# Optimization experiments

Hardware: AMD Instinct MI355X
Metric: run time of the kernel (lower is better)

## Reference

```python
import jax, jax.numpy as jnp
import numpy as np
from jax import lax

JITTER = 1e-6


def setup_inputs() -> dict:
    key = jax.random.key(0)
    ks = jax.random.split(key, 8)
    T, sd, od = 2048, 128, 64
    y = jax.random.normal(ks[0], (T, od), dtype=jnp.float32)
    # stable transition: spectral radius < 1
    A = jax.random.normal(ks[1], (sd, sd), dtype=jnp.float32) * (0.9 / np.sqrt(sd))
    C = jax.random.normal(ks[2], (od, sd), dtype=jnp.float32) / np.sqrt(sd)
    # SPD noise covariances
    Bq = jax.random.normal(ks[3], (sd, sd), dtype=jnp.float32)
    Q = (Bq @ Bq.T) / sd * 0.1 + 0.01 * jnp.eye(sd, dtype=jnp.float32)
    Br = jax.random.normal(ks[4], (od, od), dtype=jnp.float32)
    R = (Br @ Br.T) / od * 0.1 + 0.01 * jnp.eye(od, dtype=jnp.float32)
    z0 = jax.random.normal(ks[5], (sd,), dtype=jnp.float32)
    P0 = jnp.eye(sd, dtype=jnp.float32)
    return {"y": y, "A": A, "C": C, "Q": Q, "R": R, "z0": z0, "P0": P0}


def _kf(y, A, C, Q, R, z0, P0):
    sd = A.shape[0]
    od = C.shape[0]
    dt = y.dtype
    I_s = jnp.eye(sd, dtype=dt)
    jit_o = JITTER * jnp.eye(od, dtype=dt)
    log2pi = jnp.log(jnp.asarray(2.0 * np.pi, dtype=dt))

    def update(z_pred, P_pred, y_t):
        nan_mask = jnp.isnan(y_t)
        valid = ~jnp.any(nan_mask)
        y_safe = jnp.where(nan_mask, 0.0, y_t)
        innov = y_safe - C @ z_pred                      # (od,)
        S = C @ P_pred @ C.T + R + jit_o                 # S_stable (od, od)
        PCt = P_pred @ C.T                               # (sd, od)
        K = jnp.linalg.solve(S.T, PCt.T).T               # (sd, od)
        z_u = z_pred + K @ innov
        I_KC = I_s - K @ C
        P_u = I_KC @ P_pred @ I_KC.T + K @ R @ K.T
        _, logdet = jnp.linalg.slogdet(S)
        quad = innov @ jnp.linalg.solve(S, innov)
        ll_inc = -0.5 * (logdet + quad + od * log2pi)
        z = jnp.where(valid, z_u, z_pred)
        P = jnp.where(valid, P_u, P_pred)
        ll_inc = jnp.where(valid, ll_inc, jnp.zeros((), dt))
        return z, P, ll_inc

    # t = 0: no predict step, use (z0, P0) directly
    z_0, P_0, ll0 = update(z0, P0, y[0])

    def step(carry, y_t):
        z, P, ll = carry
        z_pred = A @ z
        P_pred = A @ P @ A.T + Q
        z_n, P_n, ll_inc = update(z_pred, P_pred, y_t)
        return (z_n, P_n, ll + ll_inc), (z_n, P_n)

    (_, _, log_likelihood), (zs, Ps) = lax.scan(step, (z_0, P_0, ll0), y[1:])
    states = jnp.concatenate([z_0[None], zs], axis=0)           # (T, sd)
    covariances = jnp.concatenate([P_0[None], Ps], axis=0)      # (T, sd, sd)
    return states, covariances, log_likelihood


def reference(y, A, C, Q, R, z0, P0):
    return _kf(y, A, C, Q, R, z0, P0)
```

## Files before the change

### kernel.cpp

```cpp
#include <hip/hip_runtime.h>
#include <math.h>

#define NTH 1024
#define SD 128
#define OD 64
#define PST 130
#define SST 65

#define OFF_P     0
#define OFF_T     16640
#define OFF_PCTT  16640
#define OFF_S     24960
#define OFF_L     29120
#define OFF_LINV  24960
#define OFF_KT    24960
#define OFF_SINV  33280
#define OFF_Z     37440
#define OFF_T1    37568
#define OFF_INNOV 37760
#define OFF_RED   37824
#define OFF_MISC  37888
#define LDS_FLOATS 37896

#define WS_LL    1
#define WS_LOGD  2
#define WS_Z     128
#define WS_KT    1024
#define WS_SINV  10240
#define WS_CA    16384
#define WS_QUAD  24576

#define LCH  32
#define WARM 160

#define LOG2PI_F 1.8378770664093453f
#define FREEZE_TOL 1e-5f

__launch_bounds__(NTH)
__global__ void kf_seq(const float* __restrict__ y, const float* __restrict__ A,
                       const float* __restrict__ C, const float* __restrict__ Q,
                       const float* __restrict__ R, const float* __restrict__ z0,
                       const float* __restrict__ P0, float* __restrict__ out,
                       int T, float* __restrict__ wsf, int* __restrict__ wsi) {
  extern __shared__ float lds[];
  const int tid = (int)threadIdx.x;
  const int ti = tid >> 5, tj = tid & 31;
  float* states = out;
  float* cov = out + (size_t)T * SD;

  for (int p = 0; p < 16; ++p) {
    int idx = tid + p * NTH;
    lds[OFF_P + (idx >> 7) * PST + (idx & 127)] = P0[idx];
  }
  if (tid < SD) lds[OFF_Z + tid] = z0[tid];
  if (tid == 0) { lds[OFF_MISC + 0] = 0.f; lds[OFF_MISC + 1] = 0.f; }
  __syncthreads();

  {
    int bad = 0;
    int n4 = (T * OD) >> 2;
    for (int idx = tid; idx < n4; idx += NTH) {
      float4 v = ((const float4*)y)[idx];
      if (v.x != v.x || v.y != v.y || v.z != v.z || v.w != v.w) bad = 1;
    }
    if (bad) lds[OFF_MISC + 1] = 1.f;
  }
  __syncthreads();
  const bool hasNaN = (lds[OFF_MISC + 1] != 0.f);

  float llacc = 0.f;
  float logdet_cur = 0.f;
  int tF = T;

  for (int t = 0; t < T; ++t) {
    if (t > 0) {
      {
        const int i0 = ti * 4, j0 = tj * 4;
        float acc[4][4] = {};
        for (int k = 0; k < SD; ++k) {
          float av[4], bv[4];
#pragma unroll
          for (int r = 0; r < 4; ++r) av[r] = A[(i0 + r) * SD + k];
#pragma unroll
          for (int c = 0; c < 4; ++c) bv[c] = lds[OFF_P + k * PST + j0 + c];
#pragma unroll
          for (int r = 0; r < 4; ++r)
#pragma unroll
            for (int c = 0; c < 4; ++c) acc[r][c] += av[r] * bv[c];
        }
        __syncthreads();
#pragma unroll
        for (int r = 0; r < 4; ++r)
#pragma unroll
          for (int c = 0; c < 4; ++c)
            lds[OFF_T + (i0 + r) * PST + j0 + c] = acc[r][c];
      }
      __syncthreads();
      {
        const int i0 = ti * 4, j0 = tj * 4;
        float acc[4][4] = {};
        for (int k = 0; k < SD; ++k) {
          float av[4], xv[4];
#pragma unroll
          for (int r = 0; r < 4; ++r) av[r] = A[(i0 + r) * SD + k];
#pragma unroll
          for (int c = 0; c < 4; ++c) xv[c] = lds[OFF_T + (j0 + c) * PST + k];
#pragma unroll
          for (int r = 0; r < 4; ++r)
#pragma unroll
            for (int c = 0; c < 4; ++c) acc[r][c] += av[r] * xv[c];
        }
#pragma unroll
        for (int r = 0; r < 4; ++r)
#pragma unroll
          for (int c = 0; c < 4; ++c)
            lds[OFF_P + (i0 + r) * PST + j0 + c] =
                acc[r][c] + Q[(i0 + r) * SD + j0 + c];
      }
      {
        int i = tid >> 3, s = tid & 7;
        float sum = 0.f;
        for (int kk = 0; kk < 16; ++kk) {
          int k = s * 16 + kk;
          sum += A[i * SD + k] * lds[OFF_Z + k];
        }
        sum += __shfl_xor(sum, 1);
        sum += __shfl_xor(sum, 2);
        sum += __shfl_xor(sum, 4);
        if (s == 0) lds[OFF_T1 + i] = sum;
      }
      if (tid == 0) lds[OFF_MISC + 2] = 1.f;
      __syncthreads();
    } else {
      if (tid < SD) lds[OFF_T1 + tid] = lds[OFF_Z + tid];
      if (tid == 0) lds[OFF_MISC + 2] = 1.f;
      __syncthreads();
    }

    {
      const int a0 = ti * 2, i0 = tj * 4;
      float acc[2][4] = {};
      for (int m = 0; m < SD; ++m) {
        float c0 = C[(a0 + 0) * SD + m];
        float c1 = C[(a0 + 1) * SD + m];
        float pv[4];
#pragma unroll
        for (int c = 0; c < 4; ++c) pv[c] = lds[OFF_P + m * PST + i0 + c];
#pragma unroll
        for (int c = 0; c < 4; ++c) { acc[0][c] += c0 * pv[c]; acc[1][c] += c1 * pv[c]; }
      }
#pragma unroll
      for (int r = 0; r < 2; ++r)
#pragma unroll
        for (int c = 0; c < 4; ++c)
          lds[OFF_PCTT + (a0 + r) * PST + i0 + c] = acc[r][c];
      if (tid < OD) {
        float yv = y[(size_t)t * OD + tid];
        if (yv != yv) lds[OFF_MISC + 2] = 0.f;
      }
    }
    __syncthreads();

    {
      const int a0 = ti * 2, b0 = tj * 2;
      float acc[2][2] = {};
      for (int k = 0; k < SD; ++k) {
        float c0 = C[(a0 + 0) * SD + k];
        float c1 = C[(a0 + 1) * SD + k];
        float p0 = lds[OFF_PCTT + (b0 + 0) * PST + k];
        float p1 = lds[OFF_PCTT + (b0 + 1) * PST + k];
        acc[0][0] += c0 * p0; acc[0][1] += c0 * p1;
        acc[1][0] += c1 * p0; acc[1][1] += c1 * p1;
      }
#pragma unroll
      for (int r = 0; r < 2; ++r)
#pragma unroll
        for (int c = 0; c < 2; ++c) {
          int a = a0 + r, b = b0 + c;
          lds[OFF_S + a * SST + b] =
              acc[r][c] + R[a * OD + b] + ((a == b) ? 1e-6f : 0.f);
        }
    }
    if (tid < 512) {
      int o = tid >> 3, s = tid & 7;
      float sum = 0.f;
      for (int kk = 0; kk < 16; ++kk) {
        int k = s * 16 + kk;
        sum += C[o * SD + k] * lds[OFF_T1 + k];
      }
      sum += __shfl_xor(sum, 1);
      sum += __shfl_xor(sum, 2);
      sum += __shfl_xor(sum, 4);
      if (s == 0) {
        float yv = y[(size_t)t * OD + o];
        if (yv != yv) yv = 0.f;
        lds[OFF_INNOV + o] = yv - sum;
      }
    }
    __syncthreads();

    float logdet_step = 0.f;
    for (int j = 0; j < OD; ++j) {
      float a = lds[OFF_S + j * SST + j];
      float inva = 1.0f / a;
      float irs = rsqrtf(a);
      if (tid == 0) logdet_step += logf(a);
#pragma unroll
      for (int p = 0; p < 4; ++p) {
        int idx = tid + p * NTH;
        int i = idx >> 6, k = idx & 63;
        if (i > j && k > j)
          lds[OFF_S + i * SST + k] -=
              lds[OFF_S + i * SST + j] * lds[OFF_S + k * SST + j] * inva;
        if (k == j && i >= j)
          lds[OFF_L + i * SST + j] = lds[OFF_S + i * SST + j] * irs;
      }
      __syncthreads();
    }
    if (tid == 0) logdet_cur = logdet_step;

    if (tid < OD) {
      int c = tid;
      for (int i = 0; i < c; ++i) lds[OFF_LINV + i * SST + c] = 0.f;
      for (int i = c; i < OD; ++i) {
        float s = (i == c) ? 1.f : 0.f;
        for (int j = c; j < i; ++j)
          s -= lds[OFF_L + i * SST + j] * lds[OFF_LINV + j * SST + c];
        lds[OFF_LINV + i * SST + c] = s / lds[OFF_L + i * SST + i];
      }
    }
    __syncthreads();

    {
      const int a0 = ti * 2, b0 = tj * 2;
      float acc[2][2] = {};
      for (int k = 0; k < OD; ++k) {
        float la0 = lds[OFF_LINV + k * SST + a0 + 0];
        float la1 = lds[OFF_LINV + k * SST + a0 + 1];
        float lb0 = lds[OFF_LINV + k * SST + b0 + 0];
        float lb1 = lds[OFF_LINV + k * SST + b0 + 1];
        acc[0][0] += la0 * lb0; acc[0][1] += la0 * lb1;
        acc[1][0] += la1 * lb0; acc[1][1] += la1 * lb1;
      }
#pragma unroll
      for (int r = 0; r < 2; ++r)
#pragma unroll
        for (int c = 0; c < 2; ++c)
          lds[OFF_SINV + (a0 + r) * SST + b0 + c] = acc[r][c];
    }
    __syncthreads();

    if (tid < 512) {
      int o = tid >> 3, s = tid & 7;
      float sum = 0.f;
      for (int kk = 0; kk < 8; ++kk) {
        int k = s * 8 + kk;
        sum += lds[OFF_SINV + o * SST + k] * lds[OFF_INNOV + k];
      }
      sum += __shfl_xor(sum, 1);
      sum += __shfl_xor(sum, 2);
      sum += __shfl_xor(sum, 4);
      if (s == 0) lds[OFF_RED + o] = sum * lds[OFF_INNOV + o];
    }
    {
      const int a0 = ti * 2, i0 = tj * 4;
      float acc[2][4] = {};
      for (int b = 0; b < OD; ++b) {
        float s0 = lds[OFF_SINV + (a0 + 0) * SST + b];
        float s1 = lds[OFF_SINV + (a0 + 1) * SST + b];
        float pv[4];
#pragma unroll
        for (int c = 0; c < 4; ++c) pv[c] = lds[OFF_PCTT + b * PST + i0 + c];
#pragma unroll
        for (int c = 0; c < 4; ++c) { acc[0][c] += s0 * pv[c]; acc[1][c] += s1 * pv[c]; }
      }
      __syncthreads();
#pragma unroll
      for (int r = 0; r < 2; ++r)
#pragma unroll
        for (int c = 0; c < 4; ++c)
          lds[OFF_KT + (a0 + r) * PST + i0 + c] = acc[r][c];
    }
    __syncthreads();

    const bool valid = (lds[OFF_MISC + 2] != 0.f);
    if (tid < 64) {
      float q = lds[OFF_RED + tid];
      q += __shfl_xor(q, 1);  q += __shfl_xor(q, 2);  q += __shfl_xor(q, 4);
      q += __shfl_xor(q, 8);  q += __shfl_xor(q, 16); q += __shfl_xor(q, 32);
      if (tid == 0 && valid)
        llacc += -0.5f * (logdet_step + q + OD * LOG2PI_F);
    }
    {
      int i = tid >> 3, s = tid & 7;
      float sum = 0.f;
      for (int kk = 0; kk < 8; ++kk) {
        int k = s * 8 + kk;
        sum += lds[OFF_KT + k * PST + i] * lds[OFF_INNOV + k];
      }
      sum += __shfl_xor(sum, 1);
      sum += __shfl_xor(sum, 2);
      sum += __shfl_xor(sum, 4);
      if (s == 0) {
        float zi = lds[OFF_T1 + i] + (valid ? sum : 0.f);
        lds[OFF_Z + i] = zi;
        states[(size_t)t * SD + i] = zi;
      }
    }
    {
      const int i0 = ti * 4, j0 = tj * 4;
      float acc[4][4] = {};
      for (int a = 0; a < OD; ++a) {
        float kv[4], pv[4];
#pragma unroll
        for (int r = 0; r < 4; ++r) kv[r] = lds[OFF_KT + a * PST + i0 + r];
#pragma unroll
        for (int c = 0; c < 4; ++c) pv[c] = lds[OFF_PCTT + a * PST + j0 + c];
#pragma unroll
        for (int r = 0; r < 4; ++r)
#pragma unroll
          for (int c = 0; c < 4; ++c) acc[r][c] += kv[r] * pv[c];
      }
      if (valid) {
#pragma unroll
        for (int r = 0; r < 4; ++r)
#pragma unroll
          for (int c = 0; c < 4; ++c)
            lds[OFF_P + (i0 + r) * PST + j0 + c] -= acc[r][c];
      }
    }
    __syncthreads();

    {
      float maxd = 0.f;
      float* covt = cov + (size_t)t * SD * SD;
      const float* covp = cov + (size_t)(t - 1) * SD * SD;
#pragma unroll
      for (int p = 0; p < 4; ++p) {
        int idx = tid + p * NTH;
        int base = idx * 4;
        int i = base >> 7, j = base & 127;
        float v0 = lds[OFF_P + i * PST + j + 0];
        float v1 = lds[OFF_P + i * PST + j + 1];
        float v2 = lds[OFF_P + i * PST + j + 2];
        float v3 = lds[OFF_P + i * PST + j + 3];
        covt[base + 0] = v0; covt[base + 1] = v1;
        covt[base + 2] = v2; covt[base + 3] = v3;
        if (t > 0 && !hasNaN) {
          float4 pv = ((const float4*)covp)[idx];
          maxd = fmaxf(maxd, fmaxf(fmaxf(fabsf(v0 - pv.x), fabsf(v1 - pv.y)),
                                   fmaxf(fabsf(v2 - pv.z), fabsf(v3 - pv.w))));
        }
      }
      for (int m = 1; m < 64; m <<= 1) maxd = fmaxf(maxd, __shfl_xor(maxd, m));
      if ((tid & 63) == 0) lds[OFF_RED + (tid >> 6)] = maxd;
    }
    __syncthreads();
    if (tid == 0) {
      float md = 0.f;
      for (int w = 0; w < 16; ++w) md = fmaxf(md, lds[OFF_RED + w]);
      if (t > 0 && !hasNaN && md < FREEZE_TOL) lds[OFF_MISC + 0] = 1.f;
    }
    __syncthreads();
    if (lds[OFF_MISC + 0] != 0.f) { tF = t + 1; break; }
    __syncthreads();
  }

  if (tid == 0) {
    wsi[0] = tF;
    wsf[WS_LL] = llacc;
    wsf[WS_LOGD] = logdet_cur;
  }
  if (tid < SD) wsf[WS_Z + tid] = lds[OFF_Z + tid];
  if (tF < T) {
    for (int p = 0; p < 8; ++p) {
      int idx = tid + p * NTH;
      int a = idx >> 7, i = idx & 127;
      wsf[WS_KT + idx] = lds[OFF_KT + a * PST + i];
    }
    for (int p = 0; p < 4; ++p) {
      int idx = tid + p * NTH;
      int a = idx >> 6, b = idx & 63;
      wsf[WS_SINV + idx] = lds[OFF_SINV + a * SST + b];
    }
    __syncthreads();
    for (int p = 0; p < 16; ++p) {
      int idx = tid + p * NTH;
      lds[OFF_P + (idx >> 7) * PST + (idx & 127)] = A[idx];
    }
    __syncthreads();
    {
      const int a0 = ti * 2, k0 = tj * 4;
      float acc[2][4] = {};
      for (int m = 0; m < SD; ++m) {
        float c0 = C[(a0 + 0) * SD + m];
        float c1 = C[(a0 + 1) * SD + m];
        float av[4];
#pragma unroll
        for (int cc = 0; cc < 4; ++cc) av[cc] = lds[OFF_P + m * PST + k0 + cc];
#pragma unroll
        for (int cc = 0; cc < 4; ++cc) { acc[0][cc] += c0 * av[cc]; acc[1][cc] += c1 * av[cc]; }
      }
#pragma unroll
      for (int rr = 0; rr < 2; ++rr)
#pragma unroll
        for (int cc = 0; cc < 4; ++cc)
          wsf[WS_CA + (a0 + rr) * SD + k0 + cc] = acc[rr][cc];
    }
  }
}

__launch_bounds__(512, 1)
__global__ void kf_chunk(const float* __restrict__ y, const float* __restrict__ A,
                         const float* __restrict__ wsf, const int* __restrict__ wsi,
                         float* __restrict__ out, int T) {
  __shared__ __align__(16) float zv[SD];
  __shared__ __align__(16) float vv[192];
  __shared__ __align__(16) float yb[2][OD];
  __shared__ float red[8];
  const int tid = (int)threadIdx.x;
  const int c = (int)blockIdx.x;
  const int tF = wsi[0];
  float* states = out;
  float* quad_out = (float*)wsf + WS_QUAD;

  int t_end = (c + 1) * LCH; if (t_end > T) t_end = T;
  int t_begin = c * LCH; if (t_begin < tF) t_begin = tF;
  float qacc = 0.f;

  if (t_begin < t_end) {
    int s0 = t_begin - WARM; if (s0 < tF) s0 = tF;
    const int r = tid >> 1, h = tid & 1;
    const int ki = tid >> 2, kq = tid & 3;
    const int so = tid >> 3, se = tid & 7;

    float G[64];
    if (tid < 384) {
      const float* src = (r < SD) ? (A + r * SD + h * 64)
                                  : (wsf + WS_CA + (r - SD) * SD + h * 64);
#pragma unroll
      for (int k = 0; k < 16; ++k) {
        float4 g4 = ((const float4*)src)[k];
        G[4 * k + 0] = g4.x; G[4 * k + 1] = g4.y;
        G[4 * k + 2] = g4.z; G[4 * k + 3] = g4.w;
      }
    }
    float K[16];
#pragma unroll
    for (int k = 0; k < 16; ++k) K[k] = wsf[WS_KT + (kq * 16 + k) * SD + ki];
    float Sv[8];
#pragma unroll
    for (int k = 0; k < 8; ++k) Sv[k] = wsf[WS_SINV + so * OD + se * 8 + k];

    if (tid < SD) zv[tid] = (s0 == tF) ? wsf[WS_Z + tid] : 0.f;
    if (tid < OD) yb[s0 & 1][tid] = y[(size_t)s0 * OD + tid];
    __syncthreads();

    for (int t = s0; t < t_end; ++t) {
      if (tid < 384) {
        const float* zz = zv + h * 64;
        float sum = 0.f;
#pragma unroll
        for (int k = 0; k < 16; ++k) {
          float4 z4 = ((const float4*)zz)[k];
          sum += G[4 * k + 0] * z4.x + G[4 * k + 1] * z4.y +
                 G[4 * k + 2] * z4.z + G[4 * k + 3] * z4.w;
        }
        sum += __shfl_xor(sum, 1);
        if (h == 0) vv[r] = sum;
      } else if (tid >= 448) {
        int o = tid - 448;
        if (t + 1 < t_end) yb[(t + 1) & 1][o] = y[(size_t)(t + 1) * OD + o];
      }
      __syncthreads();
      const float* ybt = yb[t & 1];
      {
        const int a0 = kq * 16;
        float sum = 0.f;
#pragma unroll
        for (int k4 = 0; k4 < 4; ++k4) {
          float4 y4 = ((const float4*)(ybt + a0))[k4];
          float4 v4 = ((const float4*)(vv + SD + a0))[k4];
          sum += K[4 * k4 + 0] * (y4.x - v4.x) + K[4 * k4 + 1] * (y4.y - v4.y) +
                 K[4 * k4 + 2] * (y4.z - v4.z) + K[4 * k4 + 3] * (y4.w - v4.w);
        }
        sum += __shfl_xor(sum, 1);
        sum += __shfl_xor(sum, 2);
        if (kq == 0) {
          float zi = vv[ki] + sum;
          zv[ki] = zi;
          if (t >= t_begin) states[(size_t)t * SD + ki] = zi;
        }
      }
      if (t >= t_begin) {
        const int b0 = se * 8;
        float sp = 0.f;
#pragma unroll
        for (int k4 = 0; k4 < 2; ++k4) {
          float4 y4 = ((const float4*)(ybt + b0))[k4];
          float4 v4 = ((const float4*)(vv + SD + b0))[k4];
          sp += Sv[4 * k4 + 0] * (y4.x - v4.x) + Sv[4 * k4 + 1] * (y4.y - v4.y) +
                Sv[4 * k4 + 2] * (y4.z - v4.z) + Sv[4 * k4 + 3] * (y4.w - v4.w);
        }
        qacc += sp * (ybt[so] - vv[SD + so]);
      }
      __syncthreads();
    }
  }

  float q = qacc;
  for (int m = 1; m < 64; m <<= 1) q += __shfl_xor(q, m);
  if ((tid & 63) == 0) red[tid >> 6] = q;
  __syncthreads();
  if (tid == 0) {
    float s = 0.f;
    for (int w = 0; w < 8; ++w) s += red[w];
    quad_out[c] = s;
  }
}

__global__ void kf_ll(const float* __restrict__ wsf, const int* __restrict__ wsi,
                      float* __restrict__ out, int T, int nchunks) {
  if (threadIdx.x == 0 && blockIdx.x == 0) {
    int tF = wsi[0];
    float ll = wsf[WS_LL];
    if (tF < T) {
      float qs = 0.f;
      for (int c = 0; c < nchunks; ++c) qs += wsf[WS_QUAD + c];
      ll += -0.5f * (qs + (float)(T - tF) * (wsf[WS_LOGD] + (float)OD * LOG2PI_F));
    }
    out[(size_t)T * SD + (size_t)T * SD * SD] = ll;
  }
}

__global__ void kf_fill(float* __restrict__ cov, const int* __restrict__ ws_tf, int T) {
  int t = (int)blockIdx.x;
  int tF = ws_tf[0];
  if (t < tF) return;
  const float4* src = (const float4*)(cov + (size_t)(tF - 1) * SD * SD);
  float4* dst = (float4*)(cov + (size_t)t * SD * SD);
#pragma unroll
  for (int p = 0; p < 16; ++p) {
    int idx = (int)threadIdx.x + p * 256;
    dst[idx] = src[idx];
  }
}

extern "C" void kernel_launch(void* const* d_in, const int* in_sizes, int n_in,
                              void* d_out, int out_size, void* d_ws, size_t ws_size,
                              hipStream_t stream) {
  const float* y  = (const float*)d_in[0];
  const float* A  = (const float*)d_in[1];
  const float* C  = (const float*)d_in[2];
  const float* Q  = (const float*)d_in[3];
  const float* R  = (const float*)d_in[4];
  const float* z0 = (const float*)d_in[5];
  const float* P0 = (const float*)d_in[6];
  float* out = (float*)d_out;
  int T = in_sizes[0] / OD;
  float* wsf = (float*)d_ws;
  int* wsi = (int*)d_ws;

  size_t ldsBytes = (size_t)LDS_FLOATS * sizeof(float);
  (void)hipFuncSetAttribute((const void*)kf_seq,
                            hipFuncAttributeMaxDynamicSharedMemorySize,
                            (int)ldsBytes);

  kf_seq<<<dim3(1), dim3(NTH), ldsBytes, stream>>>(y, A, C, Q, R, z0, P0, out, T, wsf, wsi);

  int nch = (T + LCH - 1) / LCH;
  kf_chunk<<<dim3(nch), dim3(512), 0, stream>>>(y, A, wsf, wsi, out, T);
  kf_ll<<<dim3(1), dim3(64), 0, stream>>>(wsf, wsi, out, T, nch);

  float* cov = out + (size_t)T * SD;
  kf_fill<<<dim3(T), dim3(256), 0, stream>>>(cov, wsi, T);
}
```

Measured before the change: 3.798 ms.

## Replace explicit S inverse with in-wave Cholesky and triangular solves for gain

The Cholesky factorization of S now runs within a single wavefront using wave barriers, replacing the 64 block-wide __syncthreads steps. The explicit L-inverse and S-inverse matrix products are dropped; the Kalman gain and the S^-1 innovation are obtained by forward/back substitution on 129 right-hand-side columns. S^-1 is formed only on the frozen-tail path. The inner GEMM loops are also vectorized with float4 LDS and global loads, using a padded row stride of 132. This trades many block barriers and extra matmuls for serial triangular solves on fewer threads.

```diff
diff --git a/kernel.cpp b/kernel.cpp
--- a/kernel.cpp
+++ b/kernel.cpp
@@ -4,23 +4,18 @@
 #define NTH 1024
 #define SD 128
 #define OD 64
-#define PST 130
+#define PST 132
 #define SST 65
 
 #define OFF_P     0
-#define OFF_T     16640
-#define OFF_PCTT  16640
-#define OFF_S     24960
-#define OFF_L     29120
-#define OFF_LINV  24960
-#define OFF_KT    24960
-#define OFF_SINV  33280
-#define OFF_Z     37440
-#define OFF_T1    37568
-#define OFF_INNOV 37760
-#define OFF_RED   37824
-#define OFF_MISC  37888
-#define LDS_FLOATS 37896
+#define OFF_T     16896
+#define OFF_S     33792
+#define OFF_Z     37952
+#define OFF_T1    38080
+#define OFF_INNOV 38208
+#define OFF_RED   38272
+#define OFF_MISC  38336
+#define LDS_FLOATS 38344
 
 #define WS_LL    1
 #define WS_LOGD  2
@@ -70,6 +65,7 @@
 
   float llacc = 0.f;
   float logdet_cur = 0.f;
+  float logdet_step = 0.f;
   int tF = T;
 
   for (int t = 0; t < T; ++t) {
@@ -77,45 +73,61 @@
       {
         const int i0 = ti * 4, j0 = tj * 4;
         float acc[4][4] = {};
-        for (int k = 0; k < SD; ++k) {
-          float av[4], bv[4];
-#pragma unroll
-          for (int r = 0; r < 4; ++r) av[r] = A[(i0 + r) * SD + k];
-#pragma unroll
-          for (int c = 0; c < 4; ++c) bv[c] = lds[OFF_P + k * PST + j0 + c];
+        for (int k = 0; k < SD; k += 4) {
+          float a_[4][4], p_[4][4];
+#pragma unroll
+          for (int r = 0; r < 4; ++r) {
+            float4 v = *(const float4*)&A[(i0 + r) * SD + k];
+            a_[r][0] = v.x; a_[r][1] = v.y; a_[r][2] = v.z; a_[r][3] = v.w;
+          }
+#pragma unroll
+          for (int kk = 0; kk < 4; ++kk) {
+            float4 v = *(const float4*)&lds[OFF_P + (k + kk) * PST + j0];
+            p_[kk][0] = v.x; p_[kk][1] = v.y; p_[kk][2] = v.z; p_[kk][3] = v.w;
+          }
 #pragma unroll
           for (int r = 0; r < 4; ++r)
 #pragma unroll
-            for (int c = 0; c < 4; ++c) acc[r][c] += av[r] * bv[c];
-        }
-        __syncthreads();
-#pragma unroll
-        for (int r = 0; r < 4; ++r)
-#pragma unroll
-          for (int c = 0; c < 4; ++c)
-            lds[OFF_T + (i0 + r) * PST + j0 + c] = acc[r][c];
+            for (int c = 0; c < 4; ++c)
+#pragma unroll
+              for (int kk = 0; kk < 4; ++kk) acc[r][c] += a_[r][kk] * p_[kk][c];
+        }
+#pragma unroll
+        for (int r = 0; r < 4; ++r) {
+          float4 v = {acc[r][0], acc[r][1], acc[r][2], acc[r][3]};
+          *(float4*)&lds[OFF_T + (i0 + r) * PST + j0] = v;
+        }
       }
       __syncthreads();
       {
         const int i0 = ti * 4, j0 = tj * 4;
         float acc[4][4] = {};
-        for (int k = 0; k < SD; ++k) {
-          float av[4], xv[4];
-#pragma unroll
-          for (int r = 0; r < 4; ++r) av[r] = A[(i0 + r) * SD + k];
-#pragma unroll
-          for (int c = 0; c < 4; ++c) xv[c] = lds[OFF_T + (j0 + c) * PST + k];
+        for (int k = 0; k < SD; k += 4) {
+          float x_[4][4], a_[4][4];
+#pragma unroll
+          for (int r = 0; r < 4; ++r) {
+            float4 v = *(const float4*)&lds[OFF_T + (i0 + r) * PST + k];
+            x_[r][0] = v.x; x_[r][1] = v.y; x_[r][2] = v.z; x_[r][3] = v.w;
+          }
+#pragma unroll
+          for (int c = 0; c < 4; ++c) {
+            float4 v = *(const float4*)&A[(j0 + c) * SD + k];
+            a_[c][0] = v.x; a_[c][1] = v.y; a_[c][2] = v.z; a_[c][3] = v.w;
+          }
 #pragma unroll
           for (int r = 0; r < 4; ++r)
 #pragma unroll
-            for (int c = 0; c < 4; ++c) acc[r][c] += av[r] * xv[c];
-        }
-#pragma unroll
-        for (int r = 0; r < 4; ++r)
-#pragma unroll
-          for (int c = 0; c < 4; ++c)
-            lds[OFF_P + (i0 + r) * PST + j0 + c] =
-                acc[r][c] + Q[(i0 + r) * SD + j0 + c];
+            for (int c = 0; c < 4; ++c)
+#pragma unroll
+              for (int kk = 0; kk < 4; ++kk) acc[r][c] += x_[r][kk] * a_[c][kk];
+        }
+#pragma unroll
+        for (int r = 0; r < 4; ++r) {
+          float4 q4 = *(const float4*)&Q[(i0 + r) * SD + j0];
+          float4 v = {acc[r][0] + q4.x, acc[r][1] + q4.y,
+                      acc[r][2] + q4.z, acc[r][3] + q4.w};
+          *(float4*)&lds[OFF_P + (i0 + r) * PST + j0] = v;
+        }
       }
       {
         int i = tid >> 3, s = tid & 7;
@@ -140,20 +152,30 @@
     {
       const int a0 = ti * 2, i0 = tj * 4;
       float acc[2][4] = {};
-      for (int m = 0; m < SD; ++m) {
-        float c0 = C[(a0 + 0) * SD + m];
-        float c1 = C[(a0 + 1) * SD + m];
-        float pv[4];
-#pragma unroll
-        for (int c = 0; c < 4; ++c) pv[c] = lds[OFF_P + m * PST + i0 + c];
-#pragma unroll
-        for (int c = 0; c < 4; ++c) { acc[0][c] += c0 * pv[c]; acc[1][c] += c1 * pv[c]; }
-      }
-#pragma unroll
-      for (int r = 0; r < 2; ++r)
-#pragma unroll
-        for (int c = 0; c < 4; ++c)
-          lds[OFF_PCTT + (a0 + r) * PST + i0 + c] = acc[r][c];
+      for (int m = 0; m < SD; m += 4) {
+        float c_[2][4], p_[4][4];
+#pragma unroll
+        for (int r = 0; r < 2; ++r) {
+          float4 v = *(const float4*)&C[(a0 + r) * SD + m];
+          c_[r][0] = v.x; c_[r][1] = v.y; c_[r][2] = v.z; c_[r][3] = v.w;
+        }
+#pragma unroll
+        for (int mm = 0; mm < 4; ++mm) {
+          float4 v = *(const float4*)&lds[OFF_P + (m + mm) * PST + i0];
+          p_[mm][0] = v.x; p_[mm][1] = v.y; p_[mm][2] = v.z; p_[mm][3] = v.w;
+        }
+#pragma unroll
+        for (int r = 0; r < 2; ++r)
+#pragma unroll
+          for (int c = 0; c < 4; ++c)
+#pragma unroll
+            for (int mm = 0; mm < 4; ++mm) acc[r][c] += c_[r][mm] * p_[mm][c];
+      }
+#pragma unroll
+      for (int r = 0; r < 2; ++r) {
+        float4 v = {acc[r][0], acc[r][1], acc[r][2], acc[r][3]};
+        *(float4*)&lds[OFF_T + (a0 + r) * PST + i0] = v;
+      }
       if (tid < OD) {
         float yv = y[(size_t)t * OD + tid];
         if (yv != yv) lds[OFF_MISC + 2] = 0.f;
@@ -162,23 +184,34 @@
     __syncthreads();
 
     {
-      const int a0 = ti * 2, b0 = tj * 2;
+      const int a0 = ti * 2;
       float acc[2][2] = {};
-      for (int k = 0; k < SD; ++k) {
-        float c0 = C[(a0 + 0) * SD + k];
-        float c1 = C[(a0 + 1) * SD + k];
-        float p0 = lds[OFF_PCTT + (b0 + 0) * PST + k];
-        float p1 = lds[OFF_PCTT + (b0 + 1) * PST + k];
-        acc[0][0] += c0 * p0; acc[0][1] += c0 * p1;
-        acc[1][0] += c1 * p0; acc[1][1] += c1 * p1;
+      for (int k = 0; k < SD; k += 4) {
+        float pa_[2][4], cb_[2][4];
+#pragma unroll
+        for (int r = 0; r < 2; ++r) {
+          float4 v = *(const float4*)&lds[OFF_T + (a0 + r) * PST + k];
+          pa_[r][0] = v.x; pa_[r][1] = v.y; pa_[r][2] = v.z; pa_[r][3] = v.w;
+        }
+#pragma unroll
+        for (int cb = 0; cb < 2; ++cb) {
+          float4 v = *(const float4*)&C[(tj + 32 * cb) * SD + k];
+          cb_[cb][0] = v.x; cb_[cb][1] = v.y; cb_[cb][2] = v.z; cb_[cb][3] = v.w;
+        }
+#pragma unroll
+        for (int r = 0; r < 2; ++r)
+#pragma unroll
+          for (int cb = 0; cb < 2; ++cb)
+#pragma unroll
+            for (int kk = 0; kk < 4; ++kk) acc[r][cb] += pa_[r][kk] * cb_[cb][kk];
       }
 #pragma unroll
       for (int r = 0; r < 2; ++r)
 #pragma unroll
-        for (int c = 0; c < 2; ++c) {
-          int a = a0 + r, b = b0 + c;
+        for (int cb = 0; cb < 2; ++cb) {
+          int a = a0 + r, b = tj + 32 * cb;
           lds[OFF_S + a * SST + b] =
-              acc[r][c] + R[a * OD + b] + ((a == b) ? 1e-6f : 0.f);
+              acc[r][cb] + R[a * OD + b] + ((a == b) ? 1e-6f : 0.f);
         }
     }
     if (tid < 512) {
@@ -199,104 +232,70 @@
     }
     __syncthreads();
 
-    float logdet_step = 0.f;
-    for (int j = 0; j < OD; ++j) {
-      float a = lds[OFF_S + j * SST + j];
-      float inva = 1.0f / a;
-      float irs = rsqrtf(a);
-      if (tid == 0) logdet_step += logf(a);
-#pragma unroll
-      for (int p = 0; p < 4; ++p) {
-        int idx = tid + p * NTH;
-        int i = idx >> 6, k = idx & 63;
-        if (i > j && k > j)
-          lds[OFF_S + i * SST + k] -=
-              lds[OFF_S + i * SST + j] * lds[OFF_S + k * SST + j] * inva;
-        if (k == j && i >= j)
-          lds[OFF_L + i * SST + j] = lds[OFF_S + i * SST + j] * irs;
-      }
-      __syncthreads();
-    }
-    if (tid == 0) logdet_cur = logdet_step;
-
-    if (tid < OD) {
-      int c = tid;
-      for (int i = 0; i < c; ++i) lds[OFF_LINV + i * SST + c] = 0.f;
-      for (int i = c; i < OD; ++i) {
-        float s = (i == c) ? 1.f : 0.f;
-        for (int j = c; j < i; ++j)
-          s -= lds[OFF_L + i * SST + j] * lds[OFF_LINV + j * SST + c];
-        lds[OFF_LINV + i * SST + c] = s / lds[OFF_L + i * SST + i];
-      }
-    }
-    __syncthreads();
-
-    {
-      const int a0 = ti * 2, b0 = tj * 2;
-      float acc[2][2] = {};
-      for (int k = 0; k < OD; ++k) {
-        float la0 = lds[OFF_LINV + k * SST + a0 + 0];
-        float la1 = lds[OFF_LINV + k * SST + a0 + 1];
-        float lb0 = lds[OFF_LINV + k * SST + b0 + 0];
-        float lb1 = lds[OFF_LINV + k * SST + b0 + 1];
-        acc[0][0] += la0 * lb0; acc[0][1] += la0 * lb1;
-        acc[1][0] += la1 * lb0; acc[1][1] += la1 * lb1;
-      }
-#pragma unroll
-      for (int r = 0; r < 2; ++r)
-#pragma unroll
-        for (int c = 0; c < 2; ++c)
-          lds[OFF_SINV + (a0 + r) * SST + b0 + c] = acc[r][c];
-    }
-    __syncthreads();
-
-    if (tid < 512) {
-      int o = tid >> 3, s = tid & 7;
-      float sum = 0.f;
-      for (int kk = 0; kk < 8; ++kk) {
-        int k = s * 8 + kk;
-        sum += lds[OFF_SINV + o * SST + k] * lds[OFF_INNOV + k];
-      }
-      sum += __shfl_xor(sum, 1);
-      sum += __shfl_xor(sum, 2);
-      sum += __shfl_xor(sum, 4);
-      if (s == 0) lds[OFF_RED + o] = sum * lds[OFF_INNOV + o];
-    }
-    {
-      const int a0 = ti * 2, i0 = tj * 4;
-      float acc[2][4] = {};
-      for (int b = 0; b < OD; ++b) {
-        float s0 = lds[OFF_SINV + (a0 + 0) * SST + b];
-        float s1 = lds[OFF_SINV + (a0 + 1) * SST + b];
-        float pv[4];
-#pragma unroll
-        for (int c = 0; c < 4; ++c) pv[c] = lds[OFF_PCTT + b * PST + i0 + c];
-#pragma unroll
-        for (int c = 0; c < 4; ++c) { acc[0][c] += s0 * pv[c]; acc[1][c] += s1 * pv[c]; }
-      }
-      __syncthreads();
-#pragma unroll
-      for (int r = 0; r < 2; ++r)
-#pragma unroll
-        for (int c = 0; c < 4; ++c)
-          lds[OFF_KT + (a0 + r) * PST + i0 + c] = acc[r][c];
+    logdet_step = 0.f;
+    if (tid < 64) {
+      const int i = tid;
+      for (int j = 0; j < OD; ++j) {
+        float p = lds[OFF_S + j * SST + j];
+        float inv = 1.0f / p;
+        float sij = (i > j) ? lds[OFF_S + i * SST + j] : 0.f;
+        for (int k = j + 1; k <= i; ++k) {
+          float skj = lds[OFF_S + k * SST + j];
+          lds[OFF_S + i * SST + k] -= sij * skj * inv;
+        }
+        __builtin_amdgcn_wave_barrier();
+        if (i > j) lds[OFF_S + i * SST + j] = sij * rsqrtf(p);
+        else if (i == j) lds[OFF_S + j * SST + j] = sqrtf(p);
+        if (i == 0) logdet_step += logf(p);
+        __builtin_amdgcn_wave_barrier();
+      }
+    }
+    __syncthreads();
+
+    if (tid < 129) {
+      const int c = tid;
+      const int xb = OFF_T + 64 * PST + c;
+      for (int i = 0; i < OD; ++i) {
+        float s0 = (c < SD) ? lds[OFF_T + i * PST + c] : lds[OFF_INNOV + i];
+        float s1 = 0.f;
+        int j = 0;
+        for (; j + 1 < i; j += 2) {
+          s0 -= lds[OFF_S + i * SST + j]     * lds[xb + j * PST];
+          s1 -= lds[OFF_S + i * SST + j + 1] * lds[xb + (j + 1) * PST];
+        }
+        if (j < i) s0 -= lds[OFF_S + i * SST + j] * lds[xb + j * PST];
+        lds[xb + i * PST] = (s0 + s1) / lds[OFF_S + i * SST + i];
+      }
+      for (int i = OD - 1; i >= 0; --i) {
+        float s0 = lds[xb + i * PST];
+        float s1 = 0.f;
+        int j = i + 1;
+        for (; j + 1 < OD; j += 2) {
+          s0 -= lds[OFF_S + j * SST + i]       * lds[xb + j * PST];
+          s1 -= lds[OFF_S + (j + 1) * SST + i] * lds[xb + (j + 1) * PST];
+        }
+        if (j < OD) s0 -= lds[OFF_S + j * SST + i] * lds[xb + j * PST];
+        lds[xb + i * PST] = (s0 + s1) / lds[OFF_S + i * SST + i];
+      }
     }
     __syncthreads();
 
     const bool valid = (lds[OFF_MISC + 2] != 0.f);
     if (tid < 64) {
-      float q = lds[OFF_RED + tid];
+      float q = lds[OFF_INNOV + tid] * lds[OFF_T + (64 + tid) * PST + 128];
       q += __shfl_xor(q, 1);  q += __shfl_xor(q, 2);  q += __shfl_xor(q, 4);
       q += __shfl_xor(q, 8);  q += __shfl_xor(q, 16); q += __shfl_xor(q, 32);
-      if (tid == 0 && valid)
-        llacc += -0.5f * (logdet_step + q + OD * LOG2PI_F);
+      if (tid == 0) {
+        logdet_cur = logdet_step;
+        if (valid) llacc += -0.5f * (logdet_step + q + OD * LOG2PI_F);
+      }
     }
     {
       int i = tid >> 3, s = tid & 7;
       float sum = 0.f;
       for (int kk = 0; kk < 8; ++kk) {
         int k = s * 8 + kk;
-        sum += lds[OFF_KT + k * PST + i] * lds[OFF_INNOV + k];
+        sum += lds[OFF_T + (64 + k) * PST + i] * lds[OFF_INNOV + k];
       }
       sum += __shfl_xor(sum, 1);
       sum += __shfl_xor(sum, 2);
@@ -311,22 +310,22 @@
       const int i0 = ti * 4, j0 = tj * 4;
       float acc[4][4] = {};
       for (int a = 0; a < OD; ++a) {
-        float kv[4], pv[4];
-#pragma unroll
-        for (int r = 0; r < 4; ++r) kv[r] = lds[OFF_KT + a * PST + i0 + r];
-#pragma unroll
-        for (int c = 0; c < 4; ++c) pv[c] = lds[OFF_PCTT + a * PST + j0 + c];
+        float4 kt4 = *(const float4*)&lds[OFF_T + (64 + a) * PST + i0];
+        float4 pc4 = *(const float4*)&lds[OFF_T + a * PST + j0];
+        float kt_[4] = {kt4.x, kt4.y, kt4.z, kt4.w};
+        float pc_[4] = {pc4.x, pc4.y, pc4.z, pc4.w};
 #pragma unroll
         for (int r = 0; r < 4; ++r)
 #pragma unroll
-          for (int c = 0; c < 4; ++c) acc[r][c] += kv[r] * pv[c];
+          for (int c = 0; c < 4; ++c) acc[r][c] += kt_[r] * pc_[c];
       }
       if (valid) {
 #pragma unroll
-        for (int r = 0; r < 4; ++r)
-#pragma unroll
-          for (int c = 0; c < 4; ++c)
-            lds[OFF_P + (i0 + r) * PST + j0 + c] -= acc[r][c];
+        for (int r = 0; r < 4; ++r) {
+          float4 v = *(const float4*)&lds[OFF_P + (i0 + r) * PST + j0];
+          v.x -= acc[r][0]; v.y -= acc[r][1]; v.z -= acc[r][2]; v.w -= acc[r][3];
+          *(float4*)&lds[OFF_P + (i0 + r) * PST + j0] = v;
+        }
       }
     }
     __syncthreads();
@@ -334,22 +333,17 @@
     {
       float maxd = 0.f;
       float* covt = cov + (size_t)t * SD * SD;
-      const float* covp = cov + (size_t)(t - 1) * SD * SD;
+      const float4* covp = (const float4*)(cov + (size_t)(t - 1) * SD * SD);
 #pragma unroll
       for (int p = 0; p < 4; ++p) {
         int idx = tid + p * NTH;
-        int base = idx * 4;
-        int i = base >> 7, j = base & 127;
-        float v0 = lds[OFF_P + i * PST + j + 0];
-        float v1 = lds[OFF_P + i * PST + j + 1];
-        float v2 = lds[OFF_P + i * PST + j + 2];
-        float v3 = lds[OFF_P + i * PST + j + 3];
-        covt[base + 0] = v0; covt[base + 1] = v1;
-        covt[base + 2] = v2; covt[base + 3] = v3;
+        int i = idx >> 5, j = (idx & 31) * 4;
+        float4 v = *(const float4*)&lds[OFF_P + i * PST + j];
+        ((float4*)covt)[idx] = v;
         if (t > 0 && !hasNaN) {
-          float4 pv = ((const float4*)covp)[idx];
-          maxd = fmaxf(maxd, fmaxf(fmaxf(fabsf(v0 - pv.x), fabsf(v1 - pv.y)),
-                                   fmaxf(fabsf(v2 - pv.z), fabsf(v3 - pv.w))));
+          float4 pv = covp[idx];
+          maxd = fmaxf(maxd, fmaxf(fmaxf(fabsf(v.x - pv.x), fabsf(v.y - pv.y)),
+                                   fmaxf(fabsf(v.z - pv.z), fabsf(v.w - pv.w))));
         }
       }
       for (int m = 1; m < 64; m <<= 1) maxd = fmaxf(maxd, __shfl_xor(maxd, m));
@@ -375,13 +369,27 @@
   if (tF < T) {
     for (int p = 0; p < 8; ++p) {
       int idx = tid + p * NTH;
-      int a = idx >> 7, i = idx & 127;
-      wsf[WS_KT + idx] = lds[OFF_KT + a * PST + i];
-    }
-    for (int p = 0; p < 4; ++p) {
-      int idx = tid + p * NTH;
-      int a = idx >> 6, b = idx & 63;
-      wsf[WS_SINV + idx] = lds[OFF_SINV + a * SST + b];
+      int a = idx >> 7, i2 = idx & 127;
+      wsf[WS_KT + idx] = lds[OFF_T + (64 + a) * PST + i2];
+    }
+    __syncthreads();
+    if (tid < 64) {
+      const int c = tid;
+      const int xb = OFF_T + 64 * PST + c;
+      for (int i = 0; i < OD; ++i) {
+        float s0 = (i == c) ? 1.f : 0.f;
+        for (int j = 0; j < i; ++j)
+          s0 -= lds[OFF_S + i * SST + j] * lds[xb + j * PST];
+        lds[xb + i * PST] = s0 / lds[OFF_S + i * SST + i];
+      }
+      for (int i = OD - 1; i >= 0; --i) {
+        float s0 = lds[xb + i * PST];
+        for (int j = i + 1; j < OD; ++j)
+          s0 -= lds[OFF_S + j * SST + i] * lds[xb + j * PST];
+        float xi = s0 / lds[OFF_S + i * SST + i];
+        lds[xb + i * PST] = xi;
+        wsf[WS_SINV + i * OD + c] = xi;
+      }
     }
     __syncthreads();
     for (int p = 0; p < 16; ++p) {
@@ -392,20 +400,30 @@
     {
       const int a0 = ti * 2, k0 = tj * 4;
       float acc[2][4] = {};
-      for (int m = 0; m < SD; ++m) {
-        float c0 = C[(a0 + 0) * SD + m];
-        float c1 = C[(a0 + 1) * SD + m];
-        float av[4];
-#pragma unroll
-        for (int cc = 0; cc < 4; ++cc) av[cc] = lds[OFF_P + m * PST + k0 + cc];
-#pragma unroll
-        for (int cc = 0; cc < 4; ++cc) { acc[0][cc] += c0 * av[cc]; acc[1][cc] += c1 * av[cc]; }
-      }
-#pragma unroll
-      for (int rr = 0; rr < 2; ++rr)
+      for (int m = 0; m < SD; m += 4) {
+        float c_[2][4], a_[4][4];
+#pragma unroll
+        for (int r = 0; r < 2; ++r) {
+          float4 v = *(const float4*)&C[(a0 + r) * SD + m];
+          c_[r][0] = v.x; c_[r][1] = v.y; c_[r][2] = v.z; c_[r][3] = v.w;
+        }
+#pragma unroll
+        for (int mm = 0; mm < 4; ++mm) {
+          float4 v = *(const float4*)&lds[OFF_P + (m + mm) * PST + k0];
+          a_[mm][0] = v.x; a_[mm][1] = v.y; a_[mm][2] = v.z; a_[mm][3] = v.w;
+        }
+#pragma unroll
+        for (int r = 0; r < 2; ++r)
+#pragma unroll
+          for (int cc = 0; cc < 4; ++cc)
+#pragma unroll
+            for (int mm = 0; mm < 4; ++mm) acc[r][cc] += c_[r][mm] * a_[mm][cc];
+      }
+#pragma unroll
+      for (int r = 0; r < 2; ++r)
 #pragma unroll
         for (int cc = 0; cc < 4; ++cc)
-          wsf[WS_CA + (a0 + rr) * SD + k0 + cc] = acc[rr][cc];
+          wsf[WS_CA + (a0 + r) * SD + k0 + cc] = acc[r][cc];
     }
   }
 }
```

New measurement: 5.048 ms. 32.9% more time.
